# Kernel tuning notes

Hardware: AMD Instinct MI355X
Metric: run time of the kernel (lower is better)

Reference implementation:

```python
import jax, jax.numpy as jnp
import numpy as np

BSZ, MAXQ, DH = 64, 32, 300
N_ENT, N_REL, N_TRI = 100000, 18, 600000
NUM_STEPS = 3
D_CLS = 1024


def setup_inputs() -> dict:
    key = jax.random.key(0)
    ks = jax.random.split(key, 20)
    s = 1.0 / np.sqrt(DH)
    inp = {
        "q_word_h": jax.random.normal(ks[0], (BSZ, MAXQ, DH), jnp.float32),
        "q_embeddings": jax.random.normal(ks[1], (BSZ, DH), jnp.float32),
        "e_s": jax.random.uniform(ks[2], (BSZ, N_ENT), jnp.float32),
        # per-step encoders: Linear(300,300)+Tanh, stacked over steps
        "W_step": jax.random.normal(ks[3], (NUM_STEPS, DH, DH), jnp.float32) * s,
        "b_step": jnp.zeros((NUM_STEPS, DH), jnp.float32),
        "W_cq": jax.random.normal(ks[4], (2 * DH, DH), jnp.float32) * s,
        "b_cq": jnp.zeros((DH,), jnp.float32),
        "W_ca": jax.random.normal(ks[5], (DH,), jnp.float32) * s,
        "b_ca": jnp.zeros((), jnp.float32),
        "W_rel": jax.random.normal(ks[6], (DH, N_REL), jnp.float32) * s,
        "b_rel": jnp.zeros((N_REL,), jnp.float32),
        "ent_emb": jax.random.normal(ks[7], (N_ENT, DH), jnp.float32) * s,
        "W_e1": jax.random.normal(ks[8], (DH, D_CLS), jnp.float32) * s,
        "b_e1": jnp.zeros((D_CLS,), jnp.float32),
        "W_e2": jax.random.normal(ks[9], (D_CLS, N_ENT), jnp.float32) / np.sqrt(D_CLS),
        "b_e2": jnp.zeros((N_ENT,), jnp.float32),
        # sparse KG triple lists (Msubj/Mrel/Mobj one-hot selectors)
        "subj_idx": jax.random.randint(ks[10], (N_TRI,), 0, N_ENT, jnp.int32),
        "rel_idx": jax.random.randint(ks[11], (N_TRI,), 0, N_REL, jnp.int32),
        "obj_idx": jax.random.randint(ks[12], (N_TRI,), 0, N_ENT, jnp.int32),
    }
    return inp


def _follow(e, r, subj_idx, rel_idx, obj_idx):
    # x[t, b] = e[b, subj[t]] * r[b, rel[t]];  out[b, o] = sum_{t: obj[t]=o} x[t, b]
    x = jnp.take(e, subj_idx, axis=1) * jnp.take(r, rel_idx, axis=1)  # [bsz, n_tri]
    return jax.ops.segment_sum(x.T, obj_idx, num_segments=N_ENT).T    # [bsz, n_ent]


def reference(q_word_h, q_embeddings, e_s, W_step, b_step, W_cq, b_cq, W_ca, b_ca,
              W_rel, b_rel, ent_emb, W_e1, b_e1, W_e2, b_e2,
              subj_idx, rel_idx, obj_idx):
    last_e = e_s
    last_c = jnp.zeros((q_word_h.shape[0], DH), q_word_h.dtype)
    for t in range(NUM_STEPS):
        q_t = jnp.tanh(q_embeddings @ W_step[t] + b_step[t])                 # [b, d]
        cq_t = jnp.concatenate([last_c, q_t], axis=1) @ W_cq + b_cq          # [b, d]
        # ca_linear((cq_t[:,None,:] * q_word_h)) -> logits over words
        q_logits = jnp.einsum('bd,bqd,d->bq', cq_t, q_word_h, W_ca) + b_ca   # [b, q]
        q_dist = jax.nn.softmax(q_logits, axis=1)
        last_c = jnp.einsum('bq,bqd->bd', q_dist, q_word_h)                  # attended ctx
        rel_dist = jax.nn.softmax(last_c @ W_rel + b_rel, axis=1)            # [b, n_rel]
        last_e = _follow(last_e, rel_dist, subj_idx, rel_idx, obj_idx)       # [b, n_ent]
    normed = last_e / (jnp.sum(last_e, axis=1, keepdims=True) + 1e-6)
    pred_e = normed @ ent_emb                                                # [b, d]
    pred_e = jnp.maximum(pred_e @ W_e1 + b_e1, 0.0) @ W_e2 + b_e2            # [b, n_ent]
    return pred_e
```

## Files before the change

kernel.cpp:

```cpp
#include <hip/hip_runtime.h>
#include <cstdint>

#define BSZ   64
#define MAXQ  32
#define DH    300
#define N_ENT 100000
#define N_REL 18
#define N_TRI 600000
#define D_CLS 1024

__global__ __launch_bounds__(256) void k_transpose(const float* __restrict__ e_s,
                                                   float* __restrict__ e_t) {
  __shared__ float T[64][65];
  int e0 = blockIdx.x * 64;
  int lane = threadIdx.x & 63;
  int w = threadIdx.x >> 6;
  for (int b = w; b < 64; b += 4) {
    int e = e0 + lane;
    T[b][lane] = (e < N_ENT) ? e_s[b * N_ENT + e] : 0.f;
  }
  __syncthreads();
  for (int i = w; i < 64; i += 4) {
    int e = e0 + i;
    if (e < N_ENT) e_t[e * 64 + lane] = T[lane][i];
  }
}

__global__ __launch_bounds__(256) void k_hist(const int* __restrict__ obj,
                                              int* __restrict__ cnt) {
  int stride = gridDim.x * 256;
  for (int i = blockIdx.x * 256 + threadIdx.x; i < N_TRI; i += stride)
    atomicAdd(&cnt[obj[i]], 1);
}

__global__ __launch_bounds__(256) void k_scan1(const int* __restrict__ cnt,
                                               int* __restrict__ cursor,
                                               int* __restrict__ blockSums) {
  __shared__ int sdata[256];
  int i = blockIdx.x * 256 + threadIdx.x;
  int v = (i < N_ENT) ? cnt[i] : 0;
  sdata[threadIdx.x] = v;
  __syncthreads();
  for (int off = 1; off < 256; off <<= 1) {
    int t = (threadIdx.x >= off) ? sdata[threadIdx.x - off] : 0;
    __syncthreads();
    sdata[threadIdx.x] += t;
    __syncthreads();
  }
  if (i < N_ENT) cursor[i] = sdata[threadIdx.x] - v;
  if (threadIdx.x == 255) blockSums[blockIdx.x] = sdata[255];
}

__global__ __launch_bounds__(256) void k_scan2(const int* __restrict__ blockSums,
                                               int* __restrict__ rowStart,
                                               int* __restrict__ cursor) {
  __shared__ int offs;
  int b = blockIdx.x;
  if (threadIdx.x == 0) {
    int o = 0;
    for (int j = 0; j < b; j++) o += blockSums[j];
    offs = o;
  }
  __syncthreads();
  int i = b * 256 + threadIdx.x;
  if (i < N_ENT) {
    int v = cursor[i] + offs;
    rowStart[i] = v;
    cursor[i] = v;
  }
  if (i == 0) rowStart[N_ENT] = N_TRI;
}

__global__ __launch_bounds__(256) void k_scatter(const int* __restrict__ subj,
                                                 const int* __restrict__ rel,
                                                 const int* __restrict__ obj,
                                                 int* __restrict__ cursor,
                                                 uint32_t* __restrict__ packed) {
  int stride = gridDim.x * 256;
  for (int i = blockIdx.x * 256 + threadIdx.x; i < N_TRI; i += stride) {
    int o = obj[i];
    int pos = atomicAdd(&cursor[o], 1);
    packed[pos] = (uint32_t)subj[i] | ((uint32_t)rel[i] << 17);
  }
}

__global__ __launch_bounds__(320) void k_step(
    const float* __restrict__ qwh, const float* __restrict__ qemb,
    const float* __restrict__ Wstep, const float* __restrict__ bstep,
    const float* __restrict__ Wcq, const float* __restrict__ bcq,
    const float* __restrict__ Wca, const float* __restrict__ bca,
    const float* __restrict__ Wrel, const float* __restrict__ brel,
    float* __restrict__ last_c, float* __restrict__ rel_dist, int t) {
  int b = blockIdx.x;
  int tid = threadIdx.x;
  __shared__ float qe[DH], qtL[DH], lcL[DH], wcq[DH];
  __shared__ float lg[MAXQ], red[MAXQ * 8], dist[MAXQ];
  __shared__ float relL[N_REL];
  __shared__ float mx, sm;

  for (int j = tid; j < DH; j += 320) {
    qe[j] = qemb[b * DH + j];
    lcL[j] = last_c[b * DH + j];
  }
  __syncthreads();

  const float* Wt = Wstep + t * DH * DH;
  for (int j = tid; j < DH; j += 320) {
    float acc = bstep[t * DH + j];
    for (int k = 0; k < DH; k++) acc += qe[k] * Wt[k * DH + j];
    qtL[j] = tanhf(acc);
  }
  __syncthreads();

  for (int j = tid; j < DH; j += 320) {
    float acc = bcq[j];
    for (int k = 0; k < DH; k++) acc += lcL[k] * Wcq[k * DH + j];
    for (int k = 0; k < DH; k++) acc += qtL[k] * Wcq[(DH + k) * DH + j];
    wcq[j] = acc * Wca[j];
  }
  __syncthreads();

  if (tid < MAXQ * 8) {
    int q = tid >> 3, sub = tid & 7;
    const float* row = qwh + (b * MAXQ + q) * DH;
    float acc = 0.f;
    for (int d = sub; d < DH; d += 8) acc += wcq[d] * row[d];
    red[tid] = acc;
  }
  __syncthreads();
  if (tid < MAXQ) {
    float acc = bca[0];
    for (int s = 0; s < 8; s++) acc += red[tid * 8 + s];
    lg[tid] = acc;
  }
  __syncthreads();
  if (tid == 0) {
    float m = lg[0];
    for (int q = 1; q < MAXQ; q++) m = fmaxf(m, lg[q]);
    mx = m;
  }
  __syncthreads();
  if (tid < MAXQ) dist[tid] = expf(lg[tid] - mx);
  __syncthreads();
  if (tid == 0) {
    float s = 0.f;
    for (int q = 0; q < MAXQ; q++) s += dist[q];
    sm = s;
  }
  __syncthreads();

  for (int j = tid; j < DH; j += 320) {
    float acc = 0.f;
    for (int q = 0; q < MAXQ; q++) acc += dist[q] * qwh[(b * MAXQ + q) * DH + j];
    acc /= sm;
    lcL[j] = acc;
    last_c[b * DH + j] = acc;
  }
  __syncthreads();

  if (tid < N_REL) {
    float acc = brel[tid];
    for (int d = 0; d < DH; d++) acc += lcL[d] * Wrel[d * N_REL + tid];
    relL[tid] = acc;
  }
  __syncthreads();
  if (tid == 0) {
    float m = relL[0];
    for (int r = 1; r < N_REL; r++) m = fmaxf(m, relL[r]);
    mx = m;
  }
  __syncthreads();
  if (tid < N_REL) relL[tid] = expf(relL[tid] - mx);
  __syncthreads();
  if (tid == 0) {
    float s = 0.f;
    for (int r = 0; r < N_REL; r++) s += relL[r];
    sm = s;
  }
  __syncthreads();
  if (tid < N_REL) rel_dist[b * N_REL + tid] = relL[tid] / sm;
}

__global__ __launch_bounds__(256) void k_follow(
    const float* __restrict__ e_in, const float* __restrict__ rel_dist,
    const int* __restrict__ rowStart, const uint32_t* __restrict__ packed,
    float* __restrict__ e_out, float* __restrict__ sums) {
  __shared__ float relL[BSZ * 19];
  for (int i = threadIdx.x; i < BSZ * N_REL; i += 256) {
    int l = i / N_REL, r = i - l * N_REL;
    relL[l * 19 + r] = rel_dist[i];
  }
  __syncthreads();
  int lane = threadIdx.x & 63;
  int wave = (blockIdx.x << 2) | (threadIdx.x >> 6);
  int nwaves = gridDim.x << 2;
  const float* myrel = relL + lane * 19;
  float sacc = 0.f;
  for (int o = wave; o < N_ENT; o += nwaves) {
    int beg = rowStart[o], end = rowStart[o + 1];
    float acc = 0.f;
    for (int t = beg; t < end; ++t) {
      uint32_t p = packed[t];
      int s = p & 0x1FFFF;
      int r = p >> 17;
      acc += e_in[s * 64 + lane] * myrel[r];
    }
    e_out[(size_t)o * 64 + lane] = acc;
    sacc += acc;
  }
  if (sums) atomicAdd(&sums[lane], sacc);
}

#define PF_NB 512
#define PF_EPB 196
#define PF_CH 32
#define PF_RS 304
__global__ __launch_bounds__(256) void k_predfeat(
    const float* __restrict__ e, const float* __restrict__ sums,
    const float* __restrict__ ent_emb, float* __restrict__ partials) {
  __shared__ float embL[PF_CH * PF_RS];
  __shared__ float eL[PF_CH * 64];
  int tid = threadIdx.x;
  int b = tid & 63, g = tid >> 6;
  int e0 = blockIdx.x * PF_EPB;
  int e1 = e0 + PF_EPB;
  if (e1 > N_ENT) e1 = N_ENT;

  int sb = (4 * tid) & 63;
  float4 inv4 = make_float4(1.f / (sums[sb + 0] + 1e-6f), 1.f / (sums[sb + 1] + 1e-6f),
                            1.f / (sums[sb + 2] + 1e-6f), 1.f / (sums[sb + 3] + 1e-6f));

  float4 acc[19];
  #pragma unroll
  for (int k = 0; k < 19; k++) acc[k] = make_float4(0.f, 0.f, 0.f, 0.f);

  float4* embL4 = (float4*)embL;
  float4* eL4 = (float4*)eL;

  for (int ecur = e0; ecur < e1; ecur += PF_CH) {
    int n = min(PF_CH, e1 - ecur);
    __syncthreads();
    const float4* src = (const float4*)(ent_emb + (size_t)ecur * DH);
    for (int i = tid; i < n * 75; i += 256) {
      int ee = i / 75, j = i - ee * 75;
      embL4[ee * 76 + j] = src[i];
      if (j == 0) embL4[ee * 76 + 75] = make_float4(0.f, 0.f, 0.f, 0.f);
    }
    const float4* esrc = (const float4*)(e + (size_t)ecur * 64);
    for (int i = tid; i < n * 16; i += 256) {
      float4 v = esrc[i];
      v.x *= inv4.x; v.y *= inv4.y; v.z *= inv4.z; v.w *= inv4.w;
      eL4[i] = v;
    }
    __syncthreads();
    for (int ee = 0; ee < n; ee++) {
      float ev = eL[ee * 64 + b];
      const float4* em = embL4 + ee * 76 + g * 19;
      #pragma unroll
      for (int k = 0; k < 19; k++) {
        float4 m = em[k];
        acc[k].x += ev * m.x;
        acc[k].y += ev * m.y;
        acc[k].z += ev * m.z;
        acc[k].w += ev * m.w;
      }
    }
  }

  float* pout = partials + (size_t)blockIdx.x * (PF_RS * 64);
  #pragma unroll
  for (int k = 0; k < 19; k++) {
    int d = g * 76 + k * 4;
    pout[(d + 0) * 64 + b] = acc[k].x;
    pout[(d + 1) * 64 + b] = acc[k].y;
    pout[(d + 2) * 64 + b] = acc[k].z;
    pout[(d + 3) * 64 + b] = acc[k].w;
  }
}

__global__ __launch_bounds__(256) void k_reduce_pf(const float* __restrict__ partials,
                                                   float* __restrict__ pf) {
  int j = blockIdx.x * 256 + threadIdx.x;
  if (j >= DH * 64) return;
  int d = j >> 6, b = j & 63;
  float acc = 0.f;
  for (int c = 0; c < PF_NB; c++) acc += partials[(size_t)c * (PF_RS * 64) + j];
  pf[b * DH + d] = acc;
}

__global__ __launch_bounds__(256) void k_hidden(const float* __restrict__ pf,
                                                const float* __restrict__ We1,
                                                const float* __restrict__ be1,
                                                float* __restrict__ hiddenT) {
  int idx = blockIdx.x * 256 + threadIdx.x;
  int j = idx & (D_CLS - 1);
  int b = idx >> 10;
  float acc = be1[j];
  const float* p = pf + b * DH;
  for (int k = 0; k < DH; k++) acc += p[k] * We1[k * D_CLS + j];
  hiddenT[j * 64 + b] = fmaxf(acc, 0.f);
}

#define FO_TILE 512
__global__ __launch_bounds__(256) void k_final(const float* __restrict__ hT,
                                               const float* __restrict__ We2,
                                               const float* __restrict__ be2,
                                               float* __restrict__ out) {
  int tid = threadIdx.x;
  int o0 = blockIdx.x * FO_TILE + tid * 2;
  int bg = blockIdx.y * 16;
  bool valid = (o0 < N_ENT);
  int oc = valid ? o0 : 0;

  float2 acc[16];
  #pragma unroll
  for (int i = 0; i < 16; i++) acc[i] = make_float2(0.f, 0.f);

  const float* h = hT + bg;
  const float* w = We2 + oc;
  #pragma unroll 4
  for (int k = 0; k < D_CLS; k++) {
    float2 wv = *(const float2*)(w + (size_t)k * N_ENT);
    const float* hk = h + k * 64;
    #pragma unroll
    for (int i = 0; i < 16; i++) {
      acc[i].x += hk[i] * wv.x;
      acc[i].y += hk[i] * wv.y;
    }
  }

  if (valid) {
    float2 bv = *(const float2*)(be2 + oc);
    #pragma unroll
    for (int i = 0; i < 16; i++) {
      float2 v = make_float2(acc[i].x + bv.x, acc[i].y + bv.y);
      *(float2*)(out + (size_t)(bg + i) * N_ENT + o0) = v;
    }
  }
}

extern "C" void kernel_launch(void* const* d_in, const int* in_sizes, int n_in,
                              void* d_out, int out_size, void* d_ws, size_t ws_size,
                              hipStream_t stream) {
  const float* qwh   = (const float*)d_in[0];
  const float* qemb  = (const float*)d_in[1];
  const float* e_s   = (const float*)d_in[2];
  const float* Wstep = (const float*)d_in[3];
  const float* bstep = (const float*)d_in[4];
  const float* Wcq   = (const float*)d_in[5];
  const float* bcq   = (const float*)d_in[6];
  const float* Wca   = (const float*)d_in[7];
  const float* bca   = (const float*)d_in[8];
  const float* Wrel  = (const float*)d_in[9];
  const float* brel  = (const float*)d_in[10];
  const float* eemb  = (const float*)d_in[11];
  const float* We1   = (const float*)d_in[12];
  const float* be1   = (const float*)d_in[13];
  const float* We2   = (const float*)d_in[14];
  const float* be2   = (const float*)d_in[15];
  const int* subj    = (const int*)d_in[16];
  const int* rel     = (const int*)d_in[17];
  const int* obj     = (const int*)d_in[18];
  float* out = (float*)d_out;

  float* ws = (float*)d_ws;
  const size_t EB = (size_t)N_ENT * 64;
  float* e_a      = ws;
  float* e_b      = e_a + EB;
  float* partials = e_b + EB;
  float* last_c   = partials + (size_t)PF_NB * PF_RS * 64;
  float* sums     = last_c + BSZ * DH;
  float* rel_d    = sums + 64;
  float* pf       = rel_d + BSZ * N_REL;
  float* hiddenT  = pf + BSZ * DH;
  int* cnt        = (int*)(hiddenT + BSZ * D_CLS);
  int* rowStart   = cnt + N_ENT;
  int* cursor     = rowStart + N_ENT + 1;
  int* blockSums  = cursor + N_ENT;
  uint32_t* packed = (uint32_t*)(blockSums + 400);

  hipMemsetAsync(last_c, 0, (size_t)(BSZ * DH + 64) * sizeof(float), stream);
  hipMemsetAsync(cnt, 0, (size_t)N_ENT * sizeof(int), stream);

  k_transpose<<<(N_ENT + 63) / 64, 256, 0, stream>>>(e_s, e_a);

  k_hist<<<1024, 256, 0, stream>>>(obj, cnt);
  int nsb = (N_ENT + 255) / 256;
  k_scan1<<<nsb, 256, 0, stream>>>(cnt, cursor, blockSums);
  k_scan2<<<nsb, 256, 0, stream>>>(blockSums, rowStart, cursor);
  k_scatter<<<1024, 256, 0, stream>>>(subj, rel, obj, cursor, packed);

  float* cur = e_a;
  float* nxt = e_b;
  for (int t = 0; t < 3; t++) {
    k_step<<<BSZ, 320, 0, stream>>>(qwh, qemb, Wstep, bstep, Wcq, bcq, Wca, bca,
                                    Wrel, brel, last_c, rel_d, t);
    k_follow<<<2048, 256, 0, stream>>>(cur, rel_d, rowStart, packed, nxt,
                                       (t == 2) ? sums : nullptr);
    float* tmp = cur; cur = nxt; nxt = tmp;
  }

  k_predfeat<<<PF_NB, 256, 0, stream>>>(cur, sums, eemb, partials);
  k_reduce_pf<<<(DH * 64 + 255) / 256, 256, 0, stream>>>(partials, pf);
  k_hidden<<<(BSZ * D_CLS) / 256, 256, 0, stream>>>(pf, We1, be1, hiddenT);
  dim3 fgrid((N_ENT + FO_TILE - 1) / FO_TILE, 4);
  k_final<<<fgrid, 256, 0, stream>>>(hiddenT, We2, be2, out);
}
```

Measured before the change: 1.572 ms.

## Unroll follow gather loop and restructure final GEMV to one column per thread

The sparse follow kernel's inner loop is unrolled by four so several packed-index and gathered e_in loads are in flight at once, hiding gather latency. The final W_e2 projection now gives each thread a single output column with all 64 batch rows accumulated in registers. The old layout split the batch across four grid rows, so each W_e2 element was read from global memory four times; now it is read once, using 8-deep k batches of loads. The costs are 64 accumulators per thread (more register pressure), 64-thread blocks, and uncoalesced-by-batch strided output stores.

```diff
diff --git a/kernel.cpp b/kernel.cpp
--- a/kernel.cpp
+++ b/kernel.cpp
@@ -199,11 +199,24 @@
   for (int o = wave; o < N_ENT; o += nwaves) {
     int beg = rowStart[o], end = rowStart[o + 1];
     float acc = 0.f;
-    for (int t = beg; t < end; ++t) {
+    int t = beg;
+    for (; t + 4 <= end; t += 4) {
+      uint32_t p0 = packed[t + 0];
+      uint32_t p1 = packed[t + 1];
+      uint32_t p2 = packed[t + 2];
+      uint32_t p3 = packed[t + 3];
+      float v0 = e_in[(p0 & 0x1FFFF) * 64 + lane];
+      float v1 = e_in[(p1 & 0x1FFFF) * 64 + lane];
+      float v2 = e_in[(p2 & 0x1FFFF) * 64 + lane];
+      float v3 = e_in[(p3 & 0x1FFFF) * 64 + lane];
+      acc += v0 * myrel[p0 >> 17];
+      acc += v1 * myrel[p1 >> 17];
+      acc += v2 * myrel[p2 >> 17];
+      acc += v3 * myrel[p3 >> 17];
+    }
+    for (; t < end; ++t) {
       uint32_t p = packed[t];
-      int s = p & 0x1FFFF;
-      int r = p >> 17;
-      acc += e_in[s * 64 + lane] * myrel[r];
+      acc += e_in[(p & 0x1FFFF) * 64 + lane] * myrel[p >> 17];
     }
     e_out[(size_t)o * 64 + lane] = acc;
     sacc += acc;
@@ -301,41 +314,36 @@
   hiddenT[j * 64 + b] = fmaxf(acc, 0.f);
 }
 
-#define FO_TILE 512
-__global__ __launch_bounds__(256) void k_final(const float* __restrict__ hT,
-                                               const float* __restrict__ We2,
-                                               const float* __restrict__ be2,
-                                               float* __restrict__ out) {
-  int tid = threadIdx.x;
-  int o0 = blockIdx.x * FO_TILE + tid * 2;
-  int bg = blockIdx.y * 16;
-  bool valid = (o0 < N_ENT);
-  int oc = valid ? o0 : 0;
-
-  float2 acc[16];
+__global__ __launch_bounds__(64) void k_final(const float* __restrict__ hT,
+                                              const float* __restrict__ We2,
+                                              const float* __restrict__ be2,
+                                              float* __restrict__ out) {
+  int o = blockIdx.x * 64 + threadIdx.x;
+  bool valid = (o < N_ENT);
+  int oc = valid ? o : 0;
+
+  float acc[64];
   #pragma unroll
-  for (int i = 0; i < 16; i++) acc[i] = make_float2(0.f, 0.f);
-
-  const float* h = hT + bg;
+  for (int b = 0; b < 64; b++) acc[b] = 0.f;
+
   const float* w = We2 + oc;
-  #pragma unroll 4
-  for (int k = 0; k < D_CLS; k++) {
-    float2 wv = *(const float2*)(w + (size_t)k * N_ENT);
-    const float* hk = h + k * 64;
+  for (int k0 = 0; k0 < D_CLS; k0 += 8) {
+    float wv[8];
     #pragma unroll
-    for (int i = 0; i < 16; i++) {
-      acc[i].x += hk[i] * wv.x;
-      acc[i].y += hk[i] * wv.y;
+    for (int u = 0; u < 8; u++) wv[u] = w[(size_t)(k0 + u) * N_ENT];
+    #pragma unroll
+    for (int u = 0; u < 8; u++) {
+      const float* hk = hT + (k0 + u) * 64;
+      #pragma unroll
+      for (int b = 0; b < 64; b++) acc[b] += hk[b] * wv[u];
     }
   }
 
   if (valid) {
-    float2 bv = *(const float2*)(be2 + oc);
+    float bv = be2[oc];
     #pragma unroll
-    for (int i = 0; i < 16; i++) {
-      float2 v = make_float2(acc[i].x + bv.x, acc[i].y + bv.y);
-      *(float2*)(out + (size_t)(bg + i) * N_ENT + o0) = v;
-    }
+    for (int b = 0; b < 64; b++)
+      out[(size_t)b * N_ENT + o] = acc[b] + bv;
   }
 }
 
@@ -403,6 +411,5 @@
   k_predfeat<<<PF_NB, 256, 0, stream>>>(cur, sums, eemb, partials);
   k_reduce_pf<<<(DH * 64 + 255) / 256, 256, 0, stream>>>(partials, pf);
   k_hidden<<<(BSZ * D_CLS) / 256, 256, 0, stream>>>(pf, We1, be1, hiddenT);
-  dim3 fgrid((N_ENT + FO_TILE - 1) / FO_TILE, 4);
-  k_final<<<fgrid, 256, 0, stream>>>(hiddenT, We2, be2, out);
-}
+  k_final<<<(N_ENT + 63) / 64, 64, 0, stream>>>(hiddenT, We2, be2, out);
+}
```

Result: slower. 1.613 ms (+2.6%).
